# Optimization experiments

Hardware: AMD Instinct MI355X
Metric: run time of the kernel (lower is better)

The kernel has to match this reference:

```python
import jax, jax.numpy as jnp
import numpy as np

H = 200  # LSTM units per layer
SEQ_LEN = 100
NUM_AXIS = 4


def setup_inputs() -> dict:
    key = jax.random.key(0)
    ks = jax.random.split(key, 12)
    B = 8192
    s = 0.05  # small init scale to avoid gate saturation
    inp = {
        "x": jax.random.normal(ks[0], (B, SEQ_LEN, 1), dtype=jnp.float32),
        # layer 0: input dim 1
        "W0": jax.random.normal(ks[1], (1, 4 * H), dtype=jnp.float32) * s,
        "U0": jax.random.normal(ks[2], (H, 4 * H), dtype=jnp.float32) * s,
        "b0": jax.random.normal(ks[3], (4 * H,), dtype=jnp.float32) * s,
        # layer 1
        "W1": jax.random.normal(ks[4], (H, 4 * H), dtype=jnp.float32) * s,
        "U1": jax.random.normal(ks[5], (H, 4 * H), dtype=jnp.float32) * s,
        "b1": jax.random.normal(ks[6], (4 * H,), dtype=jnp.float32) * s,
        # layer 2
        "W2": jax.random.normal(ks[7], (H, 4 * H), dtype=jnp.float32) * s,
        "U2": jax.random.normal(ks[8], (H, 4 * H), dtype=jnp.float32) * s,
        "b2": jax.random.normal(ks[9], (4 * H,), dtype=jnp.float32) * s,
        # dense head: 200 -> 400, tanh
        "Wfc": jax.random.normal(ks[10], (H, SEQ_LEN * NUM_AXIS), dtype=jnp.float32) * s,
        "bfc": jax.random.normal(ks[11], (SEQ_LEN * NUM_AXIS,), dtype=jnp.float32) * s,
    }
    return inp


def _lstm_step(h, c, xt, W, U, b):
    # Keras LSTMCell gate order: i, f, g(candidate), o
    z = xt @ W + h @ U + b  # [B, 4H]
    i, f, g, o = jnp.split(z, 4, axis=-1)
    c_new = jax.nn.sigmoid(f) * c + jax.nn.sigmoid(i) * jnp.tanh(g)
    h_new = jax.nn.sigmoid(o) * jnp.tanh(c_new)
    return h_new, c_new


def reference(x, W0, U0, b0, W1, U1, b1, W2, U2, b2, Wfc, bfc):
    B = x.shape[0]
    zeros = jnp.zeros((B, H), dtype=x.dtype)
    carry0 = (zeros, zeros, zeros, zeros, zeros, zeros)

    def step(carry, xt):
        h0, c0, h1, c1, h2, c2 = carry
        h0, c0 = _lstm_step(h0, c0, xt, W0, U0, b0)
        h1, c1 = _lstm_step(h1, c1, h0, W1, U1, b1)
        h2, c2 = _lstm_step(h2, c2, h1, W2, U2, b2)
        return (h0, c0, h1, c1, h2, c2), None

    # scan over time: x is [B, T, 1] -> [T, B, 1]
    xs = jnp.swapaxes(x, 0, 1)
    (h0, c0, h1, c1, h2, c2), _ = jax.lax.scan(step, carry0, xs)
    # return_sequences=False -> final top-layer hidden state
    y = jnp.tanh(h2 @ Wfc + bfc)  # [B, 400]
    return y.reshape(B, SEQ_LEN, NUM_AXIS)
```

## Files before the change

kernel.cpp:

```cpp
#include <hip/hip_runtime.h>

#define Hdim 200
#define NP   800
#define Tlen 100
#define BT   32
#define KB   7
#define HS   232
#define NT   50
#define THREADS 640
#define CH   5
#define CHSTR (NT*64*8)
#define MATSZ (KB*CHSTR)
#define SBUF  2560

#define WAIT_VM5   0x0F75
#define WAIT_LGKM0 0xC07F

typedef float f32x4 __attribute__((ext_vector_type(4)));
typedef short s16x8 __attribute__((ext_vector_type(8)));

__device__ __forceinline__ ushort f2bf(float f) {
    unsigned u = __float_as_uint(f);
    return (ushort)((u + 0x7fffu + ((u >> 16) & 1u)) >> 16);
}
__device__ __forceinline__ float bf2f(ushort s) {
    return __uint_as_float(((unsigned)s) << 16);
}
__device__ __forceinline__ float sigmoid_fast(float v) {
    return 1.0f / (1.0f + __expf(-v));
}
__device__ __forceinline__ float tanh_fast(float v) {
    return 2.0f / (1.0f + __expf(-2.0f * v)) - 1.0f;
}
__device__ __forceinline__ void wg_barrier() {
    asm volatile("" ::: "memory");
    __builtin_amdgcn_s_waitcnt(WAIT_LGKM0);
    __builtin_amdgcn_s_barrier();
    asm volatile("" ::: "memory");
}

__global__ void pack_weights(const float* __restrict__ U0, const float* __restrict__ W1,
                             const float* __restrict__ U1, const float* __restrict__ W2,
                             const float* __restrict__ U2, ushort* __restrict__ dst) {
    int idx = blockIdx.x * blockDim.x + threadIdx.x;
    if (idx >= 5 * KB * NT * 64) return;
    int lane = idx & 63; int rest = idx >> 6;
    int nt = rest % NT; rest /= NT;
    int kb = rest % KB; int mi = rest / KB;
    const float* src = (mi == 0) ? U0 : (mi == 1) ? W1 : (mi == 2) ? U1 : (mi == 3) ? W2 : U2;
    int np = nt * 16 + (lane & 15);
    int ncol = (np & 3) * Hdim + (np >> 2);
    int k0 = kb * 32 + (lane >> 4) * 8;
    ushort v[8];
#pragma unroll
    for (int j = 0; j < 8; ++j) {
        int k = k0 + j;
        v[j] = (k < Hdim) ? f2bf(src[k * NP + ncol]) : (ushort)0;
    }
    uint4 o;
    o.x = (unsigned)v[0] | ((unsigned)v[1] << 16);
    o.y = (unsigned)v[2] | ((unsigned)v[3] << 16);
    o.z = (unsigned)v[4] | ((unsigned)v[5] << 16);
    o.w = (unsigned)v[6] | ((unsigned)v[7] << 16);
    ((uint4*)dst)[idx] = o;
}

__device__ __forceinline__ void stage_chunk(const ushort* gp, ushort* dstbuf, int lane) {
#pragma unroll
    for (int mt = 0; mt < CH; ++mt) {
        __builtin_amdgcn_global_load_lds(
            (const __attribute__((address_space(1))) void*)(gp + (size_t)mt * 512 + lane * 8),
            (__attribute__((address_space(3))) void*)(dstbuf + mt * 512),
            16, 0, 0);
    }
}

__device__ __forceinline__ void unpack4(const ushort* p, float (&o)[4]) {
    uint2 u = *(const uint2*)p;
    o[0] = bf2f((ushort)(u.x));  o[1] = bf2f((ushort)(u.x >> 16));
    o[2] = bf2f((ushort)(u.y));  o[3] = bf2f((ushort)(u.y >> 16));
}

__device__ __forceinline__ void gate_phase(f32x4 (&acc)[2][CH],
                                           float (&creg)[2][CH],
                                           ushort* __restrict__ hbl,
                                           int lane, int ct0) {
    const int l15 = lane & 15, q = lane >> 4;
#pragma unroll
    for (int nt = 0; nt < 2; ++nt) {
#pragma unroll
        for (int mt = 0; mt < CH; ++mt) {
            const int u = (ct0 + mt) * 4 + q;
            const int n = nt * 16 + l15;
            f32x4 z = acc[nt][mt];
            float iv = sigmoid_fast(z[0]);
            float fv = sigmoid_fast(z[1]);
            float gv = tanh_fast(z[2]);
            float ov = sigmoid_fast(z[3]);
            float c = fv * creg[nt][mt] + iv * gv;
            creg[nt][mt] = c;
            hbl[n * HS + u] = f2bf(ov * tanh_fast(c));
        }
    }
}

__device__ __forceinline__ void run_slots(int s0, int s1, int t,
        ushort* __restrict__ sl, f32x4 (&acc)[2][CH],
        const ushort* __restrict__ pk, const uint* gTab, const uint* bhTab,
        const ushort* hbflat, int bhbase, int lane, int& isl) {
#pragma unroll 1
    for (int s = s0; s < s1; ++s) {
        __builtin_amdgcn_s_waitcnt(WAIT_VM5);
        ushort* buf = sl + ((t + s) & 1) * SBUF;
        s16x8 frag[CH];
#pragma unroll
        for (int mt = 0; mt < CH; ++mt)
            frag[mt] = *(const s16x8*)(buf + mt * 512 + lane * 8);
        const ushort* bp = hbflat + bhTab[s] + bhbase;
        s16x8 bh0 = *(const s16x8*)bp;
        s16x8 bh1 = *(const s16x8*)(bp + 16 * HS);
#pragma unroll
        for (int mt = 0; mt < CH; ++mt) {
            acc[0][mt] = __builtin_amdgcn_mfma_f32_16x16x32_bf16(frag[mt], bh0, acc[0][mt], 0, 0, 0);
            acc[1][mt] = __builtin_amdgcn_mfma_f32_16x16x32_bf16(frag[mt], bh1, acc[1][mt], 0, 0, 0);
        }
        __builtin_amdgcn_s_waitcnt(WAIT_LGKM0);
        stage_chunk(pk + gTab[isl], buf, lane);
        isl = (isl == 34) ? 0 : isl + 1;
    }
}

__global__ void __launch_bounds__(THREADS)
lstm3_mfma(const float* __restrict__ x,
           const float* __restrict__ W0, const float* __restrict__ b0,
           const float* __restrict__ b1, const float* __restrict__ b2,
           const float* __restrict__ Wfc, const float* __restrict__ bfc,
           const ushort* __restrict__ packed,
           float* __restrict__ out) {
    __shared__ ushort hb[3][BT][HS];
    __shared__ ushort stage[10][2][SBUF];
    __shared__ ushort pbwb[4][NP];
    __shared__ ushort xTs[Tlen][BT];
    __shared__ uint   gTab[35];
    __shared__ uint   bhTab[35];

    const int tid = threadIdx.x;
    const int wave = tid >> 6, lane = tid & 63;
    const int l15 = lane & 15, q = lane >> 4;
    const int ct0 = wave * CH;
    const int bx = blockIdx.x;
    const int bbase = bx * BT;

    for (int i = tid; i < 3 * BT * HS; i += THREADS) ((ushort*)hb)[i] = 0;
    for (int i = tid; i < NP; i += THREADS) {
        int nc = (i & 3) * Hdim + (i >> 2);
        pbwb[0][i] = f2bf(b0[nc]); pbwb[1][i] = f2bf(b1[nc]);
        pbwb[2][i] = f2bf(b2[nc]); pbwb[3][i] = f2bf(W0[nc]);
    }
    for (int i = tid; i < BT * Tlen; i += THREADS) {
        int m = i / Tlen, tt = i % Tlen;
        xTs[tt][m] = f2bf(x[(size_t)(bbase + m) * Tlen + tt]);
    }
    if (tid < 35) {
        int s = tid; uint goff, bhoff;
        if (s < 7) {
            int c = (s + bx) % 7;
            goff = 0u * MATSZ + c * CHSTR;  bhoff = 0u * BT * HS + c * 32;
        } else if (s < 14) {
            int c = (s - 7 + bx) % 7;
            goff = 2u * MATSZ + c * CHSTR;  bhoff = 1u * BT * HS + c * 32;
        } else if (s < 21) {
            int c = (s - 14 + bx) % 7;
            goff = 1u * MATSZ + c * CHSTR;  bhoff = 0u * BT * HS + c * 32;
        } else if (s < 28) {
            int c = (s - 21 + bx * 5) % 7;
            goff = 4u * MATSZ + c * CHSTR;  bhoff = 2u * BT * HS + c * 32;
        } else {
            int c = (s - 28 + bx * 5) % 7;
            goff = 3u * MATSZ + c * CHSTR;  bhoff = 1u * BT * HS + c * 32;
        }
        gTab[s] = goff; bhTab[s] = bhoff;
    }
    __syncthreads();

    float creg[3][2][CH];
#pragma unroll
    for (int l = 0; l < 3; ++l)
#pragma unroll
        for (int nt = 0; nt < 2; ++nt)
#pragma unroll
            for (int mt = 0; mt < CH; ++mt) creg[l][nt][mt] = 0.0f;

    const ushort* pk = packed + (size_t)(ct0 * 64) * 8;
    ushort* sl = &stage[wave][0][0];
    ushort* hbflat = &hb[0][0][0];
    const int bhbase = l15 * HS + q * 8;

    stage_chunk(pk + gTab[0], sl, lane);
    stage_chunk(pk + gTab[1], sl + SBUF, lane);
    int isl = 2;

    for (int t = 0; t < Tlen; ++t) {
        f32x4 acc[2][CH];

        const float xn0 = bf2f(xTs[t][l15]);
        const float xn1 = bf2f(xTs[t][16 + l15]);
#pragma unroll
        for (int mt = 0; mt < CH; ++mt) {
            const int row = (ct0 + mt) * 16 + q * 4;
            float bb[4], ww[4];
            unpack4(&pbwb[0][row], bb);
            unpack4(&pbwb[3][row], ww);
#pragma unroll
            for (int r = 0; r < 4; ++r) {
                acc[0][mt][r] = fmaf(xn0, ww[r], bb[r]);
                acc[1][mt][r] = fmaf(xn1, ww[r], bb[r]);
            }
        }

        run_slots(0, 7, t, sl, acc, pk, gTab, bhTab, hbflat, bhbase, lane, isl);
        wg_barrier();

        gate_phase(acc, creg[0], hbflat + 0 * BT * HS, lane, ct0);
#pragma unroll
        for (int mt = 0; mt < CH; ++mt) {
            const int row = (ct0 + mt) * 16 + q * 4;
            float bb[4];
            unpack4(&pbwb[1][row], bb);
#pragma unroll
            for (int r = 0; r < 4; ++r) { acc[0][mt][r] = bb[r]; acc[1][mt][r] = bb[r]; }
        }
        run_slots(7, 14, t, sl, acc, pk, gTab, bhTab, hbflat, bhbase, lane, isl);
        wg_barrier();

        run_slots(14, 21, t, sl, acc, pk, gTab, bhTab, hbflat, bhbase, lane, isl);
        gate_phase(acc, creg[1], hbflat + 1 * BT * HS, lane, ct0);
#pragma unroll
        for (int mt = 0; mt < CH; ++mt) {
            const int row = (ct0 + mt) * 16 + q * 4;
            float bb[4];
            unpack4(&pbwb[2][row], bb);
#pragma unroll
            for (int r = 0; r < 4; ++r) { acc[0][mt][r] = bb[r]; acc[1][mt][r] = bb[r]; }
        }
        run_slots(21, 28, t, sl, acc, pk, gTab, bhTab, hbflat, bhbase, lane, isl);
        wg_barrier();

        run_slots(28, 35, t, sl, acc, pk, gTab, bhTab, hbflat, bhbase, lane, isl);
        gate_phase(acc, creg[2], hbflat + 2 * BT * HS, lane, ct0);
    }
    __syncthreads();

    for (int gidx = tid; gidx < BT * 100; gidx += THREADS) {
        int m = gidx / 100;
        int j4 = (gidx % 100) * 4;
        const ushort* h2 = &hb[2][m][0];
        float4 a4 = *(const float4*)(bfc + j4);
        float s0 = a4.x, s1 = a4.y, s2 = a4.z, s3 = a4.w;
        for (int k = 0; k < Hdim; ++k) {
            float hk = bf2f(h2[k]);
            float4 w4 = *(const float4*)(Wfc + (size_t)k * 400 + j4);
            s0 = fmaf(hk, w4.x, s0);
            s1 = fmaf(hk, w4.y, s1);
            s2 = fmaf(hk, w4.z, s2);
            s3 = fmaf(hk, w4.w, s3);
        }
        float4 o4;
        o4.x = tanh_fast(s0); o4.y = tanh_fast(s1);
        o4.z = tanh_fast(s2); o4.w = tanh_fast(s3);
        *(float4*)(out + (size_t)(bbase + m) * 400 + j4) = o4;
    }
}

extern "C" void kernel_launch(void* const* d_in, const int* in_sizes, int n_in,
                              void* d_out, int out_size, void* d_ws, size_t ws_size,
                              hipStream_t stream) {
    const float* x   = (const float*)d_in[0];
    const float* W0  = (const float*)d_in[1];
    const float* U0  = (const float*)d_in[2];
    const float* b0  = (const float*)d_in[3];
    const float* W1  = (const float*)d_in[4];
    const float* U1  = (const float*)d_in[5];
    const float* b1  = (const float*)d_in[6];
    const float* W2  = (const float*)d_in[7];
    const float* U2  = (const float*)d_in[8];
    const float* b2  = (const float*)d_in[9];
    const float* Wfc = (const float*)d_in[10];
    const float* bfc = (const float*)d_in[11];
    float* out = (float*)d_out;
    ushort* packed = (ushort*)d_ws;

    const int B = in_sizes[0] / Tlen;
    const int pack_threads = 5 * KB * NT * 64;
    pack_weights<<<(pack_threads + 255) / 256, 256, 0, stream>>>(U0, W1, U1, W2, U2, packed);
    lstm3_mfma<<<B / BT, THREADS, 0, stream>>>(x, W0, b0, b1, b2, Wfc, bfc, packed, out);
}
```

Measured before the change: 2.829 ms.

## Split LSTM tiles over 12 waves with uneven chunks and reorder barriers

Raises the block from 10 to 12 waves, giving two waves 5 column tiles each and ten waves 4 each, chosen through a templated per-wave time loop. Merges the previously separate W/U slot ranges into 14-slot runs with rotated chunk order, and places barriers both before and after each gate phase instead of interleaving gate writes with the next layer's MMA slots. The aim is more wave-level parallelism and shorter per-wave serial MMA chains per timestep. The cost is extra barriers, load imbalance between 5-tile and 4-tile waves, and more register and LDS pressure per block.

```diff
diff --git a/kernel.cpp b/kernel.cpp
--- a/kernel.cpp
+++ b/kernel.cpp
@@ -7,13 +7,10 @@
 #define KB   7
 #define HS   232
 #define NT   50
-#define THREADS 640
-#define CH   5
+#define THREADS 768
 #define CHSTR (NT*64*8)
 #define MATSZ (KB*CHSTR)
-#define SBUF  2560
-
-#define WAIT_VM5   0x0F75
+
 #define WAIT_LGKM0 0xC07F
 
 typedef float f32x4 __attribute__((ext_vector_type(4)));
@@ -65,9 +62,10 @@
     ((uint4*)dst)[idx] = o;
 }
 
+template<int CHW>
 __device__ __forceinline__ void stage_chunk(const ushort* gp, ushort* dstbuf, int lane) {
 #pragma unroll
-    for (int mt = 0; mt < CH; ++mt) {
+    for (int mt = 0; mt < CHW; ++mt) {
         __builtin_amdgcn_global_load_lds(
             (const __attribute__((address_space(1))) void*)(gp + (size_t)mt * 512 + lane * 8),
             (__attribute__((address_space(3))) void*)(dstbuf + mt * 512),
@@ -81,16 +79,17 @@
     o[2] = bf2f((ushort)(u.y));  o[3] = bf2f((ushort)(u.y >> 16));
 }
 
-__device__ __forceinline__ void gate_phase(f32x4 (&acc)[2][CH],
-                                           float (&creg)[2][CH],
+template<int CHW>
+__device__ __forceinline__ void gate_phase(f32x4 (&acc)[2][CHW],
+                                           float (&creg)[2][CHW],
                                            ushort* __restrict__ hbl,
-                                           int lane, int ct0) {
+                                           int lane, int S_w) {
     const int l15 = lane & 15, q = lane >> 4;
 #pragma unroll
     for (int nt = 0; nt < 2; ++nt) {
 #pragma unroll
-        for (int mt = 0; mt < CH; ++mt) {
-            const int u = (ct0 + mt) * 4 + q;
+        for (int mt = 0; mt < CHW; ++mt) {
+            const int u = (S_w + mt) * 4 + q;
             const int n = nt * 16 + l15;
             f32x4 z = acc[nt][mt];
             float iv = sigmoid_fast(z[0]);
@@ -104,29 +103,100 @@
     }
 }
 
+template<int CHW>
 __device__ __forceinline__ void run_slots(int s0, int s1, int t,
-        ushort* __restrict__ sl, f32x4 (&acc)[2][CH],
+        ushort* __restrict__ sl, f32x4 (&acc)[2][CHW],
         const ushort* __restrict__ pk, const uint* gTab, const uint* bhTab,
         const ushort* hbflat, int bhbase, int lane, int& isl) {
 #pragma unroll 1
     for (int s = s0; s < s1; ++s) {
-        __builtin_amdgcn_s_waitcnt(WAIT_VM5);
-        ushort* buf = sl + ((t + s) & 1) * SBUF;
-        s16x8 frag[CH];
-#pragma unroll
-        for (int mt = 0; mt < CH; ++mt)
+        __builtin_amdgcn_s_waitcnt(0x0F70 | CHW);
+        ushort* buf = sl + ((t + s) & 1) * (CHW * 512);
+        s16x8 frag[CHW];
+#pragma unroll
+        for (int mt = 0; mt < CHW; ++mt)
             frag[mt] = *(const s16x8*)(buf + mt * 512 + lane * 8);
         const ushort* bp = hbflat + bhTab[s] + bhbase;
         s16x8 bh0 = *(const s16x8*)bp;
         s16x8 bh1 = *(const s16x8*)(bp + 16 * HS);
 #pragma unroll
-        for (int mt = 0; mt < CH; ++mt) {
+        for (int mt = 0; mt < CHW; ++mt) {
             acc[0][mt] = __builtin_amdgcn_mfma_f32_16x16x32_bf16(frag[mt], bh0, acc[0][mt], 0, 0, 0);
             acc[1][mt] = __builtin_amdgcn_mfma_f32_16x16x32_bf16(frag[mt], bh1, acc[1][mt], 0, 0, 0);
         }
         __builtin_amdgcn_s_waitcnt(WAIT_LGKM0);
-        stage_chunk(pk + gTab[isl], buf, lane);
+        stage_chunk<CHW>(pk + gTab[isl], buf, lane);
         isl = (isl == 34) ? 0 : isl + 1;
+    }
+}
+
+template<int CHW>
+__device__ __forceinline__ void time_loop(const int S_w, const int lane,
+        const int bhbase, ushort* __restrict__ sl, const ushort* __restrict__ pk,
+        const uint* gTab, const uint* bhTab, ushort* __restrict__ hbflat,
+        const ushort (&pbwb)[4][NP], const ushort (&xTs)[Tlen][BT]) {
+    const int l15 = lane & 15, q = lane >> 4;
+
+    float creg[3][2][CHW];
+#pragma unroll
+    for (int l = 0; l < 3; ++l)
+#pragma unroll
+        for (int nt = 0; nt < 2; ++nt)
+#pragma unroll
+            for (int mt = 0; mt < CHW; ++mt) creg[l][nt][mt] = 0.0f;
+
+    stage_chunk<CHW>(pk + gTab[0], sl, lane);
+    stage_chunk<CHW>(pk + gTab[1], sl + CHW * 512, lane);
+    int isl = 2;
+
+    for (int t = 0; t < Tlen; ++t) {
+        f32x4 acc[2][CHW];
+
+        const float xn0 = bf2f(xTs[t][l15]);
+        const float xn1 = bf2f(xTs[t][16 + l15]);
+#pragma unroll
+        for (int mt = 0; mt < CHW; ++mt) {
+            const int row = (S_w + mt) * 16 + q * 4;
+            float bb[4], ww[4];
+            unpack4(&pbwb[0][row], bb);
+            unpack4(&pbwb[3][row], ww);
+#pragma unroll
+            for (int r = 0; r < 4; ++r) {
+                acc[0][mt][r] = fmaf(xn0, ww[r], bb[r]);
+                acc[1][mt][r] = fmaf(xn1, ww[r], bb[r]);
+            }
+        }
+
+        run_slots<CHW>(0, 7, t, sl, acc, pk, gTab, bhTab, hbflat, bhbase, lane, isl);
+        wg_barrier();
+        gate_phase<CHW>(acc, creg[0], hbflat + 0 * BT * HS, lane, S_w);
+        wg_barrier();
+
+#pragma unroll
+        for (int mt = 0; mt < CHW; ++mt) {
+            const int row = (S_w + mt) * 16 + q * 4;
+            float bb[4];
+            unpack4(&pbwb[1][row], bb);
+#pragma unroll
+            for (int r = 0; r < 4; ++r) { acc[0][mt][r] = bb[r]; acc[1][mt][r] = bb[r]; }
+        }
+        run_slots<CHW>(7, 21, t, sl, acc, pk, gTab, bhTab, hbflat, bhbase, lane, isl);
+        wg_barrier();
+        gate_phase<CHW>(acc, creg[1], hbflat + 1 * BT * HS, lane, S_w);
+        wg_barrier();
+
+#pragma unroll
+        for (int mt = 0; mt < CHW; ++mt) {
+            const int row = (S_w + mt) * 16 + q * 4;
+            float bb[4];
+            unpack4(&pbwb[2][row], bb);
+#pragma unroll
+            for (int r = 0; r < 4; ++r) { acc[0][mt][r] = bb[r]; acc[1][mt][r] = bb[r]; }
+        }
+        run_slots<CHW>(21, 35, t, sl, acc, pk, gTab, bhTab, hbflat, bhbase, lane, isl);
+        wg_barrier();
+        gate_phase<CHW>(acc, creg[2], hbflat + 2 * BT * HS, lane, S_w);
+        wg_barrier();
     }
 }
 
@@ -138,7 +208,7 @@
            const ushort* __restrict__ packed,
            float* __restrict__ out) {
     __shared__ ushort hb[3][BT][HS];
-    __shared__ ushort stage[10][2][SBUF];
+    __shared__ ushort stage[NT * 1024];
     __shared__ ushort pbwb[4][NP];
     __shared__ ushort xTs[Tlen][BT];
     __shared__ uint   gTab[35];
@@ -146,8 +216,6 @@
 
     const int tid = threadIdx.x;
     const int wave = tid >> 6, lane = tid & 63;
-    const int l15 = lane & 15, q = lane >> 4;
-    const int ct0 = wave * CH;
     const int bx = blockIdx.x;
     const int bbase = bx * BT;
 
@@ -165,90 +233,29 @@
         int s = tid; uint goff, bhoff;
         if (s < 7) {
             int c = (s + bx) % 7;
-            goff = 0u * MATSZ + c * CHSTR;  bhoff = 0u * BT * HS + c * 32;
-        } else if (s < 14) {
-            int c = (s - 7 + bx) % 7;
-            goff = 2u * MATSZ + c * CHSTR;  bhoff = 1u * BT * HS + c * 32;
+            goff = 0u * MATSZ + c * CHSTR;           bhoff = 0u * BT * HS + c * 32;
         } else if (s < 21) {
-            int c = (s - 14 + bx) % 7;
-            goff = 1u * MATSZ + c * CHSTR;  bhoff = 0u * BT * HS + c * 32;
-        } else if (s < 28) {
-            int c = (s - 21 + bx * 5) % 7;
-            goff = 4u * MATSZ + c * CHSTR;  bhoff = 2u * BT * HS + c * 32;
+            int c = (s - 7 + bx) % 14;
+            if (c < 7) { goff = 2u * MATSZ + c * CHSTR;       bhoff = 1u * BT * HS + c * 32; }
+            else       { goff = 1u * MATSZ + (c - 7) * CHSTR; bhoff = 0u * BT * HS + (c - 7) * 32; }
         } else {
-            int c = (s - 28 + bx * 5) % 7;
-            goff = 3u * MATSZ + c * CHSTR;  bhoff = 1u * BT * HS + c * 32;
+            int c = (s - 21 + bx * 5) % 14;
+            if (c < 7) { goff = 4u * MATSZ + c * CHSTR;       bhoff = 2u * BT * HS + c * 32; }
+            else       { goff = 3u * MATSZ + (c - 7) * CHSTR; bhoff = 1u * BT * HS + (c - 7) * 32; }
         }
         gTab[s] = goff; bhTab[s] = bhoff;
     }
     __syncthreads();
 
-    float creg[3][2][CH];
-#pragma unroll
-    for (int l = 0; l < 3; ++l)
-#pragma unroll
-        for (int nt = 0; nt < 2; ++nt)
-#pragma unroll
-            for (int mt = 0; mt < CH; ++mt) creg[l][nt][mt] = 0.0f;
-
-    const ushort* pk = packed + (size_t)(ct0 * 64) * 8;
-    ushort* sl = &stage[wave][0][0];
+    const int S_w = (wave < 2) ? wave * 5 : 10 + (wave - 2) * 4;
+    const ushort* pk = packed + (size_t)S_w * 512;
+    ushort* sl = &stage[S_w * 1024];
     ushort* hbflat = &hb[0][0][0];
-    const int bhbase = l15 * HS + q * 8;
-
-    stage_chunk(pk + gTab[0], sl, lane);
-    stage_chunk(pk + gTab[1], sl + SBUF, lane);
-    int isl = 2;
-
-    for (int t = 0; t < Tlen; ++t) {
-        f32x4 acc[2][CH];
-
-        const float xn0 = bf2f(xTs[t][l15]);
-        const float xn1 = bf2f(xTs[t][16 + l15]);
-#pragma unroll
-        for (int mt = 0; mt < CH; ++mt) {
-            const int row = (ct0 + mt) * 16 + q * 4;
-            float bb[4], ww[4];
-            unpack4(&pbwb[0][row], bb);
-            unpack4(&pbwb[3][row], ww);
-#pragma unroll
-            for (int r = 0; r < 4; ++r) {
-                acc[0][mt][r] = fmaf(xn0, ww[r], bb[r]);
-                acc[1][mt][r] = fmaf(xn1, ww[r], bb[r]);
-            }
-        }
-
-        run_slots(0, 7, t, sl, acc, pk, gTab, bhTab, hbflat, bhbase, lane, isl);
-        wg_barrier();
-
-        gate_phase(acc, creg[0], hbflat + 0 * BT * HS, lane, ct0);
-#pragma unroll
-        for (int mt = 0; mt < CH; ++mt) {
-            const int row = (ct0 + mt) * 16 + q * 4;
-            float bb[4];
-            unpack4(&pbwb[1][row], bb);
-#pragma unroll
-            for (int r = 0; r < 4; ++r) { acc[0][mt][r] = bb[r]; acc[1][mt][r] = bb[r]; }
-        }
-        run_slots(7, 14, t, sl, acc, pk, gTab, bhTab, hbflat, bhbase, lane, isl);
-        wg_barrier();
-
-        run_slots(14, 21, t, sl, acc, pk, gTab, bhTab, hbflat, bhbase, lane, isl);
-        gate_phase(acc, creg[1], hbflat + 1 * BT * HS, lane, ct0);
-#pragma unroll
-        for (int mt = 0; mt < CH; ++mt) {
-            const int row = (ct0 + mt) * 16 + q * 4;
-            float bb[4];
-            unpack4(&pbwb[2][row], bb);
-#pragma unroll
-            for (int r = 0; r < 4; ++r) { acc[0][mt][r] = bb[r]; acc[1][mt][r] = bb[r]; }
-        }
-        run_slots(21, 28, t, sl, acc, pk, gTab, bhTab, hbflat, bhbase, lane, isl);
-        wg_barrier();
-
-        run_slots(28, 35, t, sl, acc, pk, gTab, bhTab, hbflat, bhbase, lane, isl);
-        gate_phase(acc, creg[2], hbflat + 2 * BT * HS, lane, ct0);
-    }
+    const int bhbase = (lane & 15) * HS + (lane >> 4) * 8;
+
+    if (wave < 2) time_loop<5>(S_w, lane, bhbase, sl, pk, gTab, bhTab, hbflat, pbwb, xTs);
+    else          time_loop<4>(S_w, lane, bhbase, sl, pk, gTab, bhTab, hbflat, pbwb, xTs);
+
     __syncthreads();
 
     for (int gidx = tid; gidx < BT * 100; gidx += THREADS) {
```

After: 2.644 ms, median of 2. 1.07x faster.
